# Kernel tuning notes

Measured on AMD Instinct MI355X. Metric: run time of the kernel, lower is better.

Reference implementation:

```python
import jax, jax.numpy as jnp
import numpy as np

D_MODEL = 1024
N_HEADS = 16
D_K = D_MODEL // N_HEADS


def setup_inputs() -> dict:
    key = jax.random.key(0)
    ks = jax.random.split(key, 12)
    B, S = 4, 2048
    s = 1.0 / np.sqrt(D_MODEL)
    return {
        "query": jax.random.normal(ks[0], (B, S, D_MODEL), jnp.float32),
        "key": jax.random.normal(ks[1], (B, S, D_MODEL), jnp.float32),
        "value": jax.random.normal(ks[2], (B, S, D_MODEL), jnp.float32),
        "Wq": jax.random.normal(ks[3], (D_MODEL, D_MODEL), jnp.float32) * s,
        "bq": jnp.zeros((D_MODEL,), jnp.float32),
        "Wk": jax.random.normal(ks[4], (D_MODEL, D_MODEL), jnp.float32) * s,
        "bk": jnp.zeros((D_MODEL,), jnp.float32),
        "Wv": jax.random.normal(ks[5], (D_MODEL, D_MODEL), jnp.float32) * s,
        "bv": jnp.zeros((D_MODEL,), jnp.float32),
        "Wo": jax.random.normal(ks[6], (D_MODEL, D_MODEL), jnp.float32) * s,
        "bo": jnp.zeros((D_MODEL,), jnp.float32),
    }


def reference(query, key, value, Wq, bq, Wk, bk, Wv, bv, Wo, bo):
    B, S, _ = query.shape

    def shape(x):  # [B,S,D] -> [B,H,S,d_k]
        return x.reshape(B, -1, N_HEADS, D_K).transpose(0, 2, 1, 3)

    q = shape(query @ Wq + bq)
    k = shape(key @ Wk + bk)
    v = shape(value @ Wv + bv)
    scores = jnp.einsum("bhqd,bhkd->bhqk", q, k) / jnp.sqrt(jnp.float32(D_K))
    p_attn = jax.nn.softmax(scores, axis=-1)  # dropout p=0 -> identity
    x = jnp.einsum("bhqk,bhkd->bhqd", p_attn, v)
    x = x.transpose(0, 2, 1, 3).reshape(B, -1, N_HEADS * D_K)
    return x @ Wo + bo
```

## Files before the change

kernel.cpp:

```cpp
#include <hip/hip_runtime.h>

typedef __bf16 bf16x8 __attribute__((ext_vector_type(8)));
typedef float f32x4 __attribute__((ext_vector_type(4)));
typedef float f32x16 __attribute__((ext_vector_type(16)));
typedef unsigned int u32x4v __attribute__((ext_vector_type(4)));
typedef unsigned short ushort_t;


__device__ __forceinline__ unsigned short f2bf(float f) {
    unsigned int u = __builtin_bit_cast(unsigned int, f);
    u += 0x7FFFu + ((u >> 16) & 1u);
    return (unsigned short)(u >> 16);
}

__device__ __forceinline__ unsigned int cvtpk(float lo, float hi) {
    unsigned int r;
    asm("v_cvt_pk_bf16_f32 %0, %1, %2" : "=v"(r) : "v"(lo), "v"(hi));
    return r;
}

__device__ __forceinline__ void async16(const void* g, void* l) {
    __builtin_amdgcn_global_load_lds(
        (const __attribute__((address_space(1))) void*)g,
        (__attribute__((address_space(3))) void*)l, 16, 0, 0);
}

#define MFMA16(a, b, c) __builtin_amdgcn_mfma_f32_16x16x32_bf16((a), (b), (c), 0, 0, 0)
#define MFMA32(a, b, c) __builtin_amdgcn_mfma_f32_32x32x16_bf16((a), (b), (c), 0, 0, 0)


__global__ void __launch_bounds__(256)
castk3(const float* __restrict__ a, const float* __restrict__ b, const float* __restrict__ c,
       ushort_t* __restrict__ oa, ushort_t* __restrict__ ob, ushort_t* __restrict__ oc, int n8) {
    int i = blockIdx.x * blockDim.x + threadIdx.x;
    int stride = gridDim.x * blockDim.x;
    for (; i < 3 * n8; i += stride) {
        const float* in; ushort_t* out; int j = i;
        if (j < n8)            { in = a; out = oa; }
        else if (j < 2 * n8)   { in = b; out = ob; j -= n8; }
        else                   { in = c; out = oc; j -= 2 * n8; }
        const float4* p = (const float4*)(in + (size_t)j * 8);
        float4 x = p[0], y = p[1];
        ushort_t r[8] = { f2bf(x.x), f2bf(x.y), f2bf(x.z), f2bf(x.w),
                          f2bf(y.x), f2bf(y.y), f2bf(y.z), f2bf(y.w) };
        *(uint4*)(out + (size_t)j * 8) = *(uint4*)r;
    }
}


__global__ void __launch_bounds__(256)
wtrans4(const float* __restrict__ W0, const float* __restrict__ W1,
        const float* __restrict__ W2, const float* __restrict__ W3,
        ushort_t* __restrict__ T0, ushort_t* __restrict__ T1,
        ushort_t* __restrict__ T2, ushort_t* __restrict__ T3) {
    __shared__ __attribute__((aligned(16))) float t[64][72];
    int z = blockIdx.z;
    const float* W = z == 0 ? W0 : z == 1 ? W1 : z == 2 ? W2 : W3;
    ushort_t* Wt   = z == 0 ? T0 : z == 1 ? T1 : z == 2 ? T2 : T3;
    int k0 = blockIdx.x * 64, n0 = blockIdx.y * 64;
    int tid = threadIdx.x;
#pragma unroll
    for (int i = 0; i < 4; ++i) {
        int ci = i * 256 + tid;
        int r = ci >> 4, c4 = (ci & 15) * 4;
        *(float4*)&t[r][c4] = *(const float4*)&W[(size_t)(k0 + r) * 1024 + n0 + c4];
    }
    __syncthreads();
#pragma unroll
    for (int i = 0; i < 2; ++i) {
        int ci = i * 256 + tid;
        int n = ci & 63, kb = ci >> 6;
        ushort_t tmp[8];
#pragma unroll
        for (int j = 0; j < 8; ++j) tmp[j] = f2bf(t[kb * 8 + j][n]);
        *(uint4*)&Wt[(size_t)(n0 + n) * 1024 + k0 + kb * 8] = *(uint4*)tmp;
    }
}


__global__ void __launch_bounds__(256)
vtrans(const ushort_t* __restrict__ V, ushort_t* __restrict__ Vt) {
    __shared__ __attribute__((aligned(16))) ushort_t t[64][80];
    int bh = blockIdx.x, st = blockIdx.y;
    const ushort_t* src = V + ((size_t)bh * 2048 + st * 64) * 64;
    int tid = threadIdx.x;
#pragma unroll
    for (int i = 0; i < 2; ++i) {
        int c = i * 256 + tid;
        int r = c >> 3, col = (c & 7) * 8;
        *(uint4*)&t[r][col] = *(const uint4*)&src[(size_t)r * 64 + col];
    }
    __syncthreads();
    ushort_t* dst = Vt + (size_t)bh * 64 * 2048 + st * 64;
#pragma unroll
    for (int i = 0; i < 2; ++i) {
        int c = i * 256 + tid;
        int d = c & 63, sb = c >> 6;
        ushort_t tmp[8];
#pragma unroll
        for (int j = 0; j < 8; ++j) tmp[j] = t[sb * 8 + j][d];
        *(uint4*)&dst[(size_t)d * 2048 + sb * 8] = *(uint4*)tmp;
    }
}


__global__ void __launch_bounds__(256)
proj_qkv(const ushort_t* __restrict__ Xq, const ushort_t* __restrict__ Xk,
         const ushort_t* __restrict__ Xv, const ushort_t* __restrict__ Wt,
         const float* __restrict__ bqp, const float* __restrict__ bkp,
         const float* __restrict__ bvp,
         ushort_t* __restrict__ Qp, ushort_t* __restrict__ Kp, ushort_t* __restrict__ Vp) {
    __shared__ __attribute__((aligned(16))) ushort_t lA[128 * 64];
    __shared__ __attribute__((aligned(16))) ushort_t lB[128 * 64];
    const int tid = threadIdx.x;
    const int wave = tid >> 6, lane = tid & 63;
    const int lr = lane & 15, lg = lane >> 4;
    const int wm = wave >> 1, wn = wave & 1;
    const size_t m0 = (size_t)blockIdx.x * 128;
    const int sel = blockIdx.y >> 3;
    const int n0 = (blockIdx.y & 7) * 128;

    const ushort_t* A    = sel == 0 ? Xq : sel == 1 ? Xk : Xv;
    const ushort_t* Bt   = Wt + (size_t)sel * 1024 * 1024;
    const float*    bias = sel == 0 ? bqp : sel == 1 ? bkp : bvp;
    ushort_t*       dst  = sel == 0 ? Qp : sel == 1 ? Kp : Vp;
    const float     scale = sel == 0 ? 0.18033688f : 1.0f;

    f32x4 acc[4][4] = {};

    for (int kt = 0; kt < 16; ++kt) {
        __syncthreads();
#pragma unroll
        for (int i = 0; i < 4; ++i) {
            int c = i * 256 + tid;
            int r = c >> 3;
            int sc = (c & 7) ^ (r & 7);
            async16(A + (m0 + r) * 1024 + kt * 64 + sc * 8, &lA[(i * 256 + wave * 64) * 8]);
        }
#pragma unroll
        for (int i = 0; i < 4; ++i) {
            int c = i * 256 + tid;
            int r = c >> 3;
            int sc = (c & 7) ^ (r & 7);
            async16(Bt + (size_t)(n0 + r) * 1024 + kt * 64 + sc * 8, &lB[(i * 256 + wave * 64) * 8]);
        }
        __syncthreads();
#pragma unroll
        for (int kc = 0; kc < 2; ++kc) {
            bf16x8 af[4], bfr[4];
#pragma unroll
            for (int t = 0; t < 4; ++t) {
                int rowA = wm * 64 + t * 16 + lr;
                int byteA = (rowA * 128 + (kc * 32 + lg * 8) * 2) ^ ((rowA & 7) << 4);
                af[t] = *(const bf16x8*)((const char*)lA + byteA);
                int rowB = wn * 64 + t * 16 + lr;
                int byteB = (rowB * 128 + (kc * 32 + lg * 8) * 2) ^ ((rowB & 7) << 4);
                bfr[t] = *(const bf16x8*)((const char*)lB + byteB);
            }
#pragma unroll
            for (int i = 0; i < 4; ++i)
#pragma unroll
                for (int j = 0; j < 4; ++j)
                    acc[i][j] = MFMA16(af[i], bfr[j], acc[i][j]);
        }
    }

    float bv[4];
#pragma unroll
    for (int nt = 0; nt < 4; ++nt) bv[nt] = bias[n0 + wn * 64 + nt * 16 + lr];

#pragma unroll
    for (int mt = 0; mt < 4; ++mt)
#pragma unroll
        for (int nt = 0; nt < 4; ++nt)
#pragma unroll
            for (int j = 0; j < 4; ++j) {
                size_t m = m0 + wm * 64 + mt * 16 + lg * 4 + j;
                int n = n0 + wn * 64 + nt * 16 + lr;
                size_t b = m >> 11, s = m & 2047;
                int h = n >> 6, dk = n & 63;
                float v = (acc[mt][nt][j] + bv[nt]) * scale;
                dst[((b * 16 + h) * 2048 + s) * 64 + dk] = f2bf(v);
            }
}


__global__ void __launch_bounds__(256)
gemm_out(const ushort_t* __restrict__ A, const ushort_t* __restrict__ Bt,
         const float* __restrict__ bias, float* __restrict__ dst) {
    __shared__ __attribute__((aligned(16))) ushort_t lA[128 * 64];
    __shared__ __attribute__((aligned(16))) ushort_t lB[128 * 64];
    const int tid = threadIdx.x;
    const int wave = tid >> 6, lane = tid & 63;
    const int lr = lane & 15, lg = lane >> 4;
    const int wm = wave >> 1, wn = wave & 1;
    const size_t m0 = (size_t)blockIdx.x * 128;
    const int n0 = blockIdx.y * 128;

    f32x4 acc[4][4] = {};

    for (int kt = 0; kt < 16; ++kt) {
        __syncthreads();
#pragma unroll
        for (int i = 0; i < 4; ++i) {
            int c = i * 256 + tid;
            int r = c >> 3;
            int sc = (c & 7) ^ (r & 7);
            async16(A + (m0 + r) * 1024 + kt * 64 + sc * 8, &lA[(i * 256 + wave * 64) * 8]);
        }
#pragma unroll
        for (int i = 0; i < 4; ++i) {
            int c = i * 256 + tid;
            int r = c >> 3;
            int sc = (c & 7) ^ (r & 7);
            async16(Bt + (size_t)(n0 + r) * 1024 + kt * 64 + sc * 8, &lB[(i * 256 + wave * 64) * 8]);
        }
        __syncthreads();
#pragma unroll
        for (int kc = 0; kc < 2; ++kc) {
            bf16x8 af[4], bfr[4];
#pragma unroll
            for (int t = 0; t < 4; ++t) {
                int rowA = wm * 64 + t * 16 + lr;
                int byteA = (rowA * 128 + (kc * 32 + lg * 8) * 2) ^ ((rowA & 7) << 4);
                af[t] = *(const bf16x8*)((const char*)lA + byteA);
                int rowB = wn * 64 + t * 16 + lr;
                int byteB = (rowB * 128 + (kc * 32 + lg * 8) * 2) ^ ((rowB & 7) << 4);
                bfr[t] = *(const bf16x8*)((const char*)lB + byteB);
            }
#pragma unroll
            for (int i = 0; i < 4; ++i)
#pragma unroll
                for (int j = 0; j < 4; ++j)
                    acc[i][j] = MFMA16(af[i], bfr[j], acc[i][j]);
        }
    }

    float bv[4];
#pragma unroll
    for (int nt = 0; nt < 4; ++nt) bv[nt] = bias[n0 + wn * 64 + nt * 16 + lr];

#pragma unroll
    for (int mt = 0; mt < 4; ++mt)
#pragma unroll
        for (int nt = 0; nt < 4; ++nt)
#pragma unroll
            for (int j = 0; j < 4; ++j) {
                size_t m = m0 + wm * 64 + mt * 16 + lg * 4 + j;
                int n = n0 + wn * 64 + nt * 16 + lr;
                dst[m * 1024 + n] = acc[mt][nt][j] + bv[nt];
            }
}


__global__ void __launch_bounds__(256)
attn(const ushort_t* __restrict__ Q, const ushort_t* __restrict__ Kb,
     const ushort_t* __restrict__ Vt, ushort_t* __restrict__ X) {
    __shared__ __attribute__((aligned(16))) ushort_t lK[2][4096];
    __shared__ __attribute__((aligned(16))) ushort_t lV[2][4096];
    const int tid = threadIdx.x, wave = tid >> 6, lane = tid & 63;
    const int ql = lane & 31, hi = lane >> 5;
    const int bh = blockIdx.x;
    const int q0 = blockIdx.y * 128 + wave * 32;

    const ushort_t* Qg = Q + ((size_t)bh * 2048 + q0 + ql) * 64 + hi * 8;
    bf16x8 qf[4];
#pragma unroll
    for (int dk = 0; dk < 4; ++dk) qf[dk] = *(const bf16x8*)(Qg + dk * 16);

    int offq[4];
#pragma unroll
    for (int dk = 0; dk < 4; ++dk) offq[dk] = (dk * 2 + hi) * 1024 + ql * 16;

    int gs[2], gr[2];
#pragma unroll
    for (int i = 0; i < 2; ++i) {
        int g = i * 256 + tid;
        gs[i] = g >> 6;
        gr[i] = g & 63;
    }
    const ushort_t* Kroot = Kb + (size_t)bh * 2048 * 64;
    const ushort_t* Vroot = Vt + (size_t)bh * 64 * 2048;

    auto stage = [&](int tile, int bi) {
        int kv0 = tile * 64;
#pragma unroll
        for (int i = 0; i < 2; ++i)
            async16(Kroot + (size_t)(kv0 + gr[i]) * 64 + gs[i] * 8,
                    &lK[bi][(i * 256 + wave * 64) * 8]);
#pragma unroll
        for (int i = 0; i < 2; ++i)
            async16(Vroot + (size_t)gr[i] * 2048 + kv0 + gs[i] * 8,
                    &lV[bi][(i * 256 + wave * 64) * 8]);
    };

    f32x16 oa0 = {}, oa1 = {};
    float lrun = 0.f;

    stage(0, 0);
    for (int t = 0; t < 32; ++t) {
        const int cur = t & 1;
        stage((t + 1) & 31, cur ^ 1);
        asm volatile("s_waitcnt vmcnt(4)" ::: "memory");
        __builtin_amdgcn_s_barrier();

        const char* kb = (const char*)&lK[cur][0];
        const char* vb = (const char*)&lV[cur][0];

        f32x16 st0 = {}, st1 = {};
        __builtin_amdgcn_s_setprio(1);
#pragma unroll
        for (int dk = 0; dk < 4; ++dk) {
            bf16x8 k0 = *(const bf16x8*)(kb + offq[dk]);
            bf16x8 k1 = *(const bf16x8*)(kb + offq[dk] + 512);
            st0 = MFMA32(k0, qf[dk], st0);
            st1 = MFMA32(k1, qf[dk], st1);
        }
        __builtin_amdgcn_s_setprio(0);

#pragma unroll
        for (int r = 0; r < 16; ++r) st0[r] = __builtin_amdgcn_exp2f(st0[r]);
#pragma unroll
        for (int r = 0; r < 16; ++r) st1[r] = __builtin_amdgcn_exp2f(st1[r]);
        float sa[8];
#pragma unroll
        for (int r = 0; r < 8; ++r) sa[r] = (st0[r] + st0[r + 8]) + (st1[r] + st1[r + 8]);
#pragma unroll
        for (int s = 4; s > 0; s >>= 1)
#pragma unroll
            for (int r = 0; r < s; ++r) sa[r] += sa[r + s];
        lrun += sa[0];

        bf16x8 pb[4];
#pragma unroll
        for (int ks = 0; ks < 4; ++ks) {
            int rb = (ks & 1) * 8;
            unsigned int A_, B_, C_, D_;
            if (ks < 2) {
                A_ = cvtpk(st0[rb + 0], st0[rb + 1]);
                B_ = cvtpk(st0[rb + 4], st0[rb + 5]);
                C_ = cvtpk(st0[rb + 2], st0[rb + 3]);
                D_ = cvtpk(st0[rb + 6], st0[rb + 7]);
            } else {
                A_ = cvtpk(st1[rb + 0], st1[rb + 1]);
                B_ = cvtpk(st1[rb + 4], st1[rb + 5]);
                C_ = cvtpk(st1[rb + 2], st1[rb + 3]);
                D_ = cvtpk(st1[rb + 6], st1[rb + 7]);
            }
            asm("v_permlane32_swap_b32 %0, %1" : "+v"(A_), "+v"(B_));
            asm("v_permlane32_swap_b32 %0, %1" : "+v"(C_), "+v"(D_));
            u32x4v w = { A_, C_, B_, D_ };
            pb[ks] = __builtin_bit_cast(bf16x8, w);
        }

        __builtin_amdgcn_s_setprio(1);
#pragma unroll
        for (int ks = 0; ks < 4; ++ks) {
            bf16x8 v0 = *(const bf16x8*)(vb + offq[ks]);
            bf16x8 v1 = *(const bf16x8*)(vb + offq[ks] + 512);
            oa0 = MFMA32(v0, pb[ks], oa0);
            oa1 = MFMA32(v1, pb[ks], oa1);
        }
        __builtin_amdgcn_s_setprio(0);

        __builtin_amdgcn_s_barrier();
    }

    float lt = lrun + __shfl_xor(lrun, 32);
    float inv = 1.f / lt;
    const int b = bh >> 4, h = bh & 15;
    ushort_t* dst = X + (((size_t)b * 2048 + q0 + ql) * 16 + h) * 64;
#pragma unroll
    for (int rq = 0; rq < 4; ++rq) {
        ushort_t t0[4], t1[4];
#pragma unroll
        for (int j = 0; j < 4; ++j) {
            t0[j] = f2bf(oa0[rq * 4 + j] * inv);
            t1[j] = f2bf(oa1[rq * 4 + j] * inv);
        }
        *(ushort4*)(dst + rq * 8 + hi * 4)      = *(ushort4*)t0;
        *(ushort4*)(dst + 32 + rq * 8 + hi * 4) = *(ushort4*)t1;
    }
}


extern "C" void kernel_launch(void* const* d_in, const int* in_sizes, int n_in,
                              void* d_out, int out_size, void* d_ws, size_t ws_size,
                              hipStream_t stream) {
    const float* query = (const float*)d_in[0];
    const float* key   = (const float*)d_in[1];
    const float* value = (const float*)d_in[2];
    const float* Wq = (const float*)d_in[3];
    const float* bq = (const float*)d_in[4];
    const float* Wk = (const float*)d_in[5];
    const float* bk = (const float*)d_in[6];
    const float* Wv = (const float*)d_in[7];
    const float* bv = (const float*)d_in[8];
    const float* Wo = (const float*)d_in[9];
    const float* bo = (const float*)d_in[10];
    float* out = (float*)d_out;

    char* ws = (char*)d_ws;
    const size_t MB = 1024 * 1024;
    ushort_t* Wqt = (ushort_t*)(ws + 0 * MB);
    ushort_t* Wkt = (ushort_t*)(ws + 2 * MB);
    ushort_t* Wvt = (ushort_t*)(ws + 4 * MB);
    ushort_t* Wot = (ushort_t*)(ws + 6 * MB);
    ushort_t* Xq  = (ushort_t*)(ws + 8 * MB);
    ushort_t* Xk  = (ushort_t*)(ws + 24 * MB);
    ushort_t* Xv  = (ushort_t*)(ws + 40 * MB);
    ushort_t* Qp  = (ushort_t*)(ws + 56 * MB);
    ushort_t* Kp  = (ushort_t*)(ws + 72 * MB);
    ushort_t* Vp  = (ushort_t*)(ws + 88 * MB);
    ushort_t* Vtp = Xq;
    ushort_t* Xat = Xk;

    const int n8 = 8192 * 1024 / 8;
    castk3<<<dim3(2048), dim3(256), 0, stream>>>(query, key, value, Xq, Xk, Xv, n8);

    wtrans4<<<dim3(16, 16, 4), dim3(256), 0, stream>>>(Wq, Wk, Wv, Wo, Wqt, Wkt, Wvt, Wot);

    proj_qkv<<<dim3(64, 24), dim3(256), 0, stream>>>(Xq, Xk, Xv, Wqt, bq, bk, bv, Qp, Kp, Vp);

    vtrans<<<dim3(64, 32), dim3(256), 0, stream>>>(Vp, Vtp);

    attn<<<dim3(64, 16), dim3(256), 0, stream>>>(Qp, Kp, Vtp, Xat);

    gemm_out<<<dim3(64, 8), dim3(256), 0, stream>>>(Xat, Wot, bo, out);
}
```

Before: 383.4 us.

## Pre-tile K and transposed V into LDS-order blocks for contiguous async loads

The QKV projection now writes K directly in a tiled layout matching the attention kernel's LDS staging order. The V transpose kernel writes 64x64 tiles contiguously in the same order. The attention kernel's async global-to-LDS loads therefore read one contiguous 8 KB chunk per tile instead of strided rows, which is meant to improve coalescing. The cost is scattered 2-byte stores in the projection epilogue for K and tighter coupling between the three kernels' layouts.

```diff
diff --git a/kernel.cpp b/kernel.cpp
--- a/kernel.cpp
+++ b/kernel.cpp
@@ -91,7 +91,7 @@
         *(uint4*)&t[r][col] = *(const uint4*)&src[(size_t)r * 64 + col];
     }
     __syncthreads();
-    ushort_t* dst = Vt + (size_t)bh * 64 * 2048 + st * 64;
+    ushort_t* dst = Vt + (size_t)bh * 131072 + (size_t)st * 4096;
 #pragma unroll
     for (int i = 0; i < 2; ++i) {
         int c = i * 256 + tid;
@@ -99,7 +99,7 @@
         ushort_t tmp[8];
 #pragma unroll
         for (int j = 0; j < 8; ++j) tmp[j] = t[sb * 8 + j][d];
-        *(uint4*)&dst[(size_t)d * 2048 + sb * 8] = *(uint4*)tmp;
+        *(uint4*)&dst[(size_t)c * 8] = *(uint4*)tmp;
     }
 }
 
@@ -180,7 +180,13 @@
                 size_t b = m >> 11, s = m & 2047;
                 int h = n >> 6, dk = n & 63;
                 float v = (acc[mt][nt][j] + bv[nt]) * scale;
-                dst[((b * 16 + h) * 2048 + s) * 64 + dk] = f2bf(v);
+                size_t bh = b * 16 + h;
+                if (sel == 1) {
+                    dst[bh * 131072 + (s >> 6) * 4096 + (size_t)(dk >> 3) * 512
+                        + (s & 63) * 8 + (dk & 7)] = f2bf(v);
+                } else {
+                    dst[(bh * 2048 + s) * 64 + dk] = f2bf(v);
+                }
             }
 }
 
@@ -272,26 +278,18 @@
 #pragma unroll
     for (int dk = 0; dk < 4; ++dk) offq[dk] = (dk * 2 + hi) * 1024 + ql * 16;
 
-    int gs[2], gr[2];
-#pragma unroll
-    for (int i = 0; i < 2; ++i) {
-        int g = i * 256 + tid;
-        gs[i] = g >> 6;
-        gr[i] = g & 63;
-    }
-    const ushort_t* Kroot = Kb + (size_t)bh * 2048 * 64;
-    const ushort_t* Vroot = Vt + (size_t)bh * 64 * 2048;
+    const ushort_t* Kroot = Kb + (size_t)bh * 131072;
+    const ushort_t* Vroot = Vt + (size_t)bh * 131072;
 
     auto stage = [&](int tile, int bi) {
-        int kv0 = tile * 64;
+        const ushort_t* Kt = Kroot + tile * 4096;
+        const ushort_t* Vb = Vroot + tile * 4096;
 #pragma unroll
         for (int i = 0; i < 2; ++i)
-            async16(Kroot + (size_t)(kv0 + gr[i]) * 64 + gs[i] * 8,
-                    &lK[bi][(i * 256 + wave * 64) * 8]);
+            async16(Kt + (size_t)(i * 256 + tid) * 8, &lK[bi][(i * 256 + wave * 64) * 8]);
 #pragma unroll
         for (int i = 0; i < 2; ++i)
-            async16(Vroot + (size_t)gr[i] * 2048 + kv0 + gs[i] * 8,
-                    &lV[bi][(i * 256 + wave * 64) * 8]);
+            async16(Vb + (size_t)(i * 256 + tid) * 8, &lV[bi][(i * 256 + wave * 64) * 8]);
     };
 
     f32x16 oa0 = {}, oa1 = {};
```

Result: faster. 355.6 us (-7.3%).
